# Kernel tuning notes

Hardware: AMD Instinct MI355X
Metric: run time of the kernel (lower is better)

Reference implementation:

```python
import jax, jax.numpy as jnp
import numpy as np

N, E, B, PG = 20000, 320000, 20, 1000  # nodes, edges, graphs, nodes-per-graph
H, L, NB, EI = 256, 6, 16, 8           # hidden, layers, node_base_dim, edge_in_dim
LN_EPS = 1e-5


def setup_inputs() -> dict:
    key = jax.random.key(0)
    ks = jax.random.split(key, 32)
    w = lambda i, s: (jax.random.normal(ks[i], s, jnp.float32) * 0.05)
    inp = {
        "x": jax.random.normal(ks[0], (N, NB), jnp.float32),
        "edge_attr": jax.random.normal(ks[1], (E, EI), jnp.float32),
        "c": jax.random.normal(ks[2], (B, PG), jnp.float32),
        "edge_index": jax.random.randint(ks[3], (2, E), 0, N),
        "node_gid": jnp.arange(N) // PG,   # batch.batch
        "node_lid": jnp.arange(N) % PG,    # node local index
        # edge_mlp: Linear(EI,H), ReLU, Linear(H,H)
        "ew1": w(4, (EI, H)), "eb1": jnp.zeros((H,), jnp.float32),
        "ew2": w(5, (H, H)),  "eb2": jnp.zeros((H,), jnp.float32),
        # input_proj: Linear(NB+1, H), SiLU
        "in_w": w(6, (NB + 1, H)), "in_b": jnp.zeros((H,), jnp.float32),
        # per-layer GINEConv edge lin (edge_dim -> in_channels)
        "lin_w": w(7, (L, H, H)), "lin_b": jnp.zeros((L, H), jnp.float32),
        # per-layer conv MLP: Linear(H,H), SiLU, Linear(H,H)
        "cw1": w(8, (L, H, H)), "cb1": jnp.zeros((L, H), jnp.float32),
        "cw2": w(9, (L, H, H)), "cb2": jnp.zeros((L, H), jnp.float32),
        # per-layer LayerNorm
        "ln_g": jnp.ones((L, H), jnp.float32), "ln_b": jnp.zeros((L, H), jnp.float32),
        # pool_attn: Linear(H,H), Tanh, Linear(H,1)
        "pa_w1": w(10, (H, H)), "pa_b1": jnp.zeros((H,), jnp.float32),
        "pa_w2": w(11, (H, 1)), "pa_b2": jnp.zeros((1,), jnp.float32),
        # head: Linear(H,H), SiLU, Linear(H,1)
        "hw1": w(12, (H, H)), "hb1": jnp.zeros((H,), jnp.float32),
        "hw2": w(13, (H, 1)), "hb2": jnp.zeros((1,), jnp.float32),
    }
    return inp


def _layer_norm(z, g, b):
    m = jnp.mean(z, axis=-1, keepdims=True)
    v = jnp.mean(jnp.square(z - m), axis=-1, keepdims=True)
    return (z - m) * jax.lax.rsqrt(v + LN_EPS) * g + b


def reference(x, edge_attr, c, edge_index, node_gid, node_lid,
              ew1, eb1, ew2, eb2, in_w, in_b,
              lin_w, lin_b, cw1, cb1, cw2, cb2, ln_g, ln_b,
              pa_w1, pa_b1, pa_w2, pa_b2, hw1, hb1, hw2, hb2):
    silu = jax.nn.silu
    # c_scalar: per-node coefficient
    c_scalar = c[node_gid, node_lid][:, None]                       # [N,1]
    xin = jnp.concatenate([x, c_scalar], axis=-1)                   # [N,NB+1]
    e = jax.nn.relu(edge_attr @ ew1 + eb1) @ ew2 + eb2              # [E,H]
    h = silu(xin @ in_w + in_b)                                     # [N,H]
    src, dst = edge_index[0], edge_index[1]
    for l in range(L):
        msg = jax.nn.relu(h[src] + (e @ lin_w[l] + lin_b[l]))       # [E,H]
        agg = jnp.zeros_like(h).at[dst].add(msg)                    # scatter-add
        z = h + agg                                                 # (1+eps)*x_i + agg, eps=0
        h_new = silu(z @ cw1[l] + cb1[l]) @ cw2[l] + cb2[l]
        h_new = _layer_norm(h_new, ln_g[l], ln_b[l])
        h = h + silu(h_new)
    # attention pooling: global softmax over nodes, renormalized per graph
    scores = jnp.tanh(h @ pa_w1 + pa_b1) @ pa_w2 + pa_b2            # [N,1]
    attn = jax.nn.softmax(scores, axis=0)                           # [N,1]
    seg_sum = jax.ops.segment_sum(attn[:, 0], node_gid, num_segments=B)  # [B]
    attn_n = attn[:, 0] / (seg_sum[node_gid] + 1e-8)                # [N]
    pooled = jax.ops.segment_sum(h * attn_n[:, None], node_gid, num_segments=B)  # [B,H]
    q = (silu(pooled @ hw1 + hb1) @ hw2 + hb2)[:, 0]                # [B]
    return q
```

## Files before the change

kernel.cpp:

```cpp
#include <hip/hip_runtime.h>
#include <hip/hip_bf16.h>
#include <cstdint>


#define NN 20000
#define EE 320000
#define BBG 20
#define PGN 1000
#define HH 256
#define LL 6

typedef short bf16x8 __attribute__((ext_vector_type(8)));
typedef float f32x4 __attribute__((ext_vector_type(4)));

__device__ __forceinline__ void async16(const void* g, void* l) {
  __builtin_amdgcn_global_load_lds(
      (const __attribute__((address_space(1))) unsigned int*)(uintptr_t)g,
      (__attribute__((address_space(3))) unsigned int*)(uintptr_t)l, 16, 0, 0);
}

__device__ __forceinline__ float siluf(float x) { return x / (1.f + __expf(-x)); }

__device__ __forceinline__ unsigned int f2bu(float x) {
  __hip_bfloat16 h = __float2bfloat16(x);
  return (unsigned int)*(unsigned short*)&h;
}

__device__ __forceinline__ float b2f(unsigned short u) {
  unsigned int v = ((unsigned int)u) << 16;
  return *(float*)&v;
}

enum { EPI_SILU = 1, EPI_PLAIN = 2, EPI_TANH = 3 };

template <int EPI>
__global__ void __launch_bounds__(256, 2) gemm256(
    const __hip_bfloat16* __restrict__ A, const __hip_bfloat16* __restrict__ Wt,
    const float* __restrict__ bias, int M, float* __restrict__ outf,
    __hip_bfloat16* __restrict__ outb) {
  __shared__ __align__(16) __hip_bfloat16 sA[128 * 32];
  __shared__ __align__(16) __hip_bfloat16 sB[128 * 32];

  const int t = threadIdx.x;
  const int wave = t >> 6, lane = t & 63;
  const int row0 = blockIdx.x * 128;
  const int col0 = blockIdx.y * 128;

  const int wrow = (wave >> 1) * 64;
  const int wcol = (wave & 1) * 64;
  const int fr = lane & 15, q = lane >> 4;

  f32x4 zero = {0.f, 0.f, 0.f, 0.f};
  f32x4 acc[4][4];
#pragma unroll
  for (int i = 0; i < 4; i++)
#pragma unroll
    for (int j = 0; j < 4; j++) acc[i][j] = zero;

  const int c1 = t, c2 = t + 256;
  const int lr1 = c1 >> 2, lr2 = c2 >> 2;
  const int q1 = (c1 & 3) ^ ((lr1 >> 1) & 3);
  const int q2 = (c2 & 3) ^ ((lr2 >> 1) & 3);
  int rA1 = row0 + lr1; if (rA1 >= M) rA1 = M - 1;
  int rA2 = row0 + lr2; if (rA2 >= M) rA2 = M - 1;
  const int rB1 = col0 + lr1, rB2 = col0 + lr2;

  for (int k0 = 0; k0 < 256; k0 += 32) {
    async16((const char*)(A + (size_t)rA1 * HH + k0) + q1 * 16,
            (char*)sA + wave * 1024);
    async16((const char*)(A + (size_t)rA2 * HH + k0) + q2 * 16,
            (char*)sA + 4096 + wave * 1024);
    async16((const char*)(Wt + (size_t)rB1 * HH + k0) + q1 * 16,
            (char*)sB + wave * 1024);
    async16((const char*)(Wt + (size_t)rB2 * HH + k0) + q2 * 16,
            (char*)sB + 4096 + wave * 1024);
    __syncthreads();
    bf16x8 af[4], bfr[4];
#pragma unroll
    for (int i = 0; i < 4; i++) {
      const int row = wrow + i * 16 + fr;
      af[i] = *(const bf16x8*)&sA[row * 32 + ((q ^ ((row >> 1) & 3))) * 8];
    }
#pragma unroll
    for (int j = 0; j < 4; j++) {
      const int row = wcol + j * 16 + fr;
      bfr[j] = *(const bf16x8*)&sB[row * 32 + ((q ^ ((row >> 1) & 3))) * 8];
    }
#pragma unroll
    for (int i = 0; i < 4; i++)
#pragma unroll
      for (int j = 0; j < 4; j++)
        acc[i][j] = __builtin_amdgcn_mfma_f32_16x16x32_bf16(af[i], bfr[j],
                                                            acc[i][j], 0, 0, 0);
    __syncthreads();
  }

#pragma unroll
  for (int j = 0; j < 4; j++) {
    const int col = col0 + wcol + j * 16 + fr;
    const float bs = bias[col];
#pragma unroll
    for (int i = 0; i < 4; i++) {
      const int lr0 = wrow + i * 16 + q * 4;
#pragma unroll
      for (int r = 0; r < 4; r++) {
        const int grow = row0 + lr0 + r;
        float v = acc[i][j][r] + bs;
        if (grow < M) {
          if (EPI == EPI_SILU) {
            outb[(size_t)grow * HH + col] = __float2bfloat16(siluf(v));
          } else if (EPI == EPI_PLAIN) {
            outf[(size_t)grow * HH + col] = v;
          } else {
            outb[(size_t)grow * HH + col] = __float2bfloat16(tanhf(v));
          }
        }
      }
    }
  }
}

__global__ void __launch_bounds__(256, 4) mlp_ln(
    const float* __restrict__ z, const __hip_bfloat16* __restrict__ W1t,
    const float* __restrict__ b1, const __hip_bfloat16* __restrict__ W2t,
    const float* __restrict__ b2, const float* __restrict__ g,
    const float* __restrict__ bbv, float* __restrict__ h,
    float* __restrict__ yzf, __hip_bfloat16* __restrict__ hb) {
  __shared__ __align__(16) char smem[2048 + 16384 + 32 * 264 * 2];
  __hip_bfloat16* sA = (__hip_bfloat16*)smem;
  __hip_bfloat16* sB = (__hip_bfloat16*)(smem + 2048);
  unsigned short* sT = (unsigned short*)(smem + 18432);

  const int t = threadIdx.x;
  const int wave = t >> 6, lane = t & 63;
  const int row0 = blockIdx.x * 32;
  const int fr = lane & 15, q = lane >> 4;
  const int rt = wave & 1;
  const int chf = wave >> 1;

  const int lrA = t >> 2;
  const int qA = (t & 3) ^ ((lrA >> 1) & 3);
  int qB[4], rB[4];
#pragma unroll
  for (int p = 0; p < 4; p++) {
    const int c = t + p * 256;
    const int lr = c >> 2;
    qB[p] = (c & 3) ^ ((lr >> 1) & 3);
    rB[p] = lr;
  }

  f32x4 zero = {0.f, 0.f, 0.f, 0.f};
  f32x4 acc[8];
#pragma unroll
  for (int j = 0; j < 8; j++) acc[j] = zero;

  const int arow = rt * 16 + fr;
  const int aswz = (q ^ ((arow >> 1) & 3)) * 8;

  for (int k0 = 0; k0 < 256; k0 += 32) {
    if (t < 128) {
      const float* s1 = z + (size_t)(row0 + lrA) * HH + k0 + qA * 8;
      float4 a0 = *(const float4*)s1;
      float4 a1 = *(const float4*)(s1 + 4);
      uint4 u;
      u.x = f2bu(a0.x) | (f2bu(a0.y) << 16);
      u.y = f2bu(a0.z) | (f2bu(a0.w) << 16);
      u.z = f2bu(a1.x) | (f2bu(a1.y) << 16);
      u.w = f2bu(a1.z) | (f2bu(a1.w) << 16);
      *(uint4*)((char*)sA + t * 16) = u;
    }
#pragma unroll
    for (int p = 0; p < 4; p++)
      async16((const char*)(W1t + (size_t)rB[p] * HH + k0) + qB[p] * 16,
              (char*)sB + p * 4096 + wave * 1024);
    __syncthreads();
    bf16x8 af = *(const bf16x8*)&sA[arow * 32 + aswz];
#pragma unroll
    for (int j = 0; j < 8; j++) {
      const int row = chf * 128 + j * 16 + fr;
      bf16x8 bfr = *(const bf16x8*)&sB[row * 32 + ((q ^ ((row >> 1) & 3))) * 8];
      acc[j] = __builtin_amdgcn_mfma_f32_16x16x32_bf16(af, bfr, acc[j], 0, 0, 0);
    }
    __syncthreads();
  }
#pragma unroll
  for (int j = 0; j < 8; j++) {
    const int col = chf * 128 + j * 16 + fr;
    const float bs = b1[col];
    const int r0 = rt * 16 + q * 4;
#pragma unroll
    for (int r = 0; r < 4; r++)
      sT[(r0 + r) * 264 + col] = (unsigned short)f2bu(siluf(acc[j][r] + bs));
  }
#pragma unroll
  for (int j = 0; j < 8; j++) acc[j] = zero;

  for (int k0 = 0; k0 < 256; k0 += 32) {
#pragma unroll
    for (int p = 0; p < 4; p++)
      async16((const char*)(W2t + (size_t)rB[p] * HH + k0) + qB[p] * 16,
              (char*)sB + p * 4096 + wave * 1024);
    __syncthreads();
    bf16x8 af = *(const bf16x8*)&sT[arow * 264 + k0 + q * 8];
#pragma unroll
    for (int j = 0; j < 8; j++) {
      const int row = chf * 128 + j * 16 + fr;
      bf16x8 bfr = *(const bf16x8*)&sB[row * 32 + ((q ^ ((row >> 1) & 3))) * 8];
      acc[j] = __builtin_amdgcn_mfma_f32_16x16x32_bf16(af, bfr, acc[j], 0, 0, 0);
    }
    __syncthreads();
  }
#pragma unroll
  for (int j = 0; j < 8; j++) {
    const int col = chf * 128 + j * 16 + fr;
    const float bs = b2[col];
    const int r0 = rt * 16 + q * 4;
#pragma unroll
    for (int r = 0; r < 4; r++)
      sT[(r0 + r) * 264 + col] = (unsigned short)f2bu(acc[j][r] + bs);
  }
  __syncthreads();

  for (int rr = 0; rr < 8; rr++) {
    const int r = wave * 8 + rr;
    const int grow = row0 + r;
    float v[4];
    float s = 0.f;
#pragma unroll
    for (int i = 0; i < 4; i++) {
      v[i] = b2f(sT[r * 264 + lane + i * 64]);
      s += v[i];
    }
#pragma unroll
    for (int o = 32; o; o >>= 1) s += __shfl_xor(s, o);
    const float mean = s * (1.f / 256.f);
    float var = 0.f;
#pragma unroll
    for (int i = 0; i < 4; i++) { float d = v[i] - mean; var += d * d; }
#pragma unroll
    for (int o = 32; o; o >>= 1) var += __shfl_xor(var, o);
    const float rs = rsqrtf(var * (1.f / 256.f) + 1e-5f);
#pragma unroll
    for (int i = 0; i < 4; i++) {
      const int c = lane + i * 64;
      float ln = (v[i] - mean) * rs * g[c] + bbv[c];
      float si = siluf(ln);
      size_t idx = (size_t)grow * HH + c;
      float nh = h[idx] + si;
      h[idx] = nh;
      yzf[idx] = nh;
      hb[idx] = __float2bfloat16(nh);
    }
  }
}

__global__ void __launch_bounds__(256, 4) edge_fused(
    const __hip_bfloat16* __restrict__ te, const __hip_bfloat16* __restrict__ Wt,
    const float* __restrict__ bias, const __hip_bfloat16* __restrict__ hbv,
    const int* __restrict__ srcp, const int* __restrict__ dstp,
    float* __restrict__ z) {
  __shared__ __align__(16) char smem[32768];
  __shared__ int sSrc[128], sDst[128];
  __hip_bfloat16* sA = (__hip_bfloat16*)smem;
  __hip_bfloat16* sB = (__hip_bfloat16*)(smem + 16384);
  unsigned short* sRed = (unsigned short*)smem;

  const int t = threadIdx.x;
  const int wave = t >> 6, lane = t & 63;
  const int row0 = blockIdx.y * 128;
  const int col0 = blockIdx.x * 128;

  if (t < 128) { sSrc[t] = srcp[row0 + t]; sDst[t] = dstp[row0 + t]; }
  __syncthreads();

  const int wrow = (wave >> 1) * 64;
  const int fr = lane & 15, q = lane >> 4;
  const int rc = lane, rb = wave;

  f32x4 zero = {0.f, 0.f, 0.f, 0.f};
  f32x4 acc[4][4];
#pragma unroll
  for (int i = 0; i < 4; i++)
#pragma unroll
    for (int j = 0; j < 4; j++) acc[i][j] = zero;

  const int c1 = t, c2 = t + 256;
  const int lr1 = c1 >> 2, lr2 = c2 >> 2;
  const int q1 = (c1 & 3) ^ ((lr1 >> 1) & 3);
  const int q2 = (c2 & 3) ^ ((lr2 >> 1) & 3);
  const int rA1 = row0 + lr1, rA2 = row0 + lr2;
  const int rB1 = col0 + lr1, rB2 = col0 + lr2;

#pragma unroll
  for (int it = 0; it < 4; it++) {
    const int ka = it * 64, kb = ka + 32;
    async16((const char*)(te + (size_t)rA1 * HH + ka) + q1 * 16,
            (char*)sA + wave * 1024);
    async16((const char*)(te + (size_t)rA2 * HH + ka) + q2 * 16,
            (char*)sA + 4096 + wave * 1024);
    async16((const char*)(te + (size_t)rA1 * HH + kb) + q1 * 16,
            (char*)sA + 8192 + wave * 1024);
    async16((const char*)(te + (size_t)rA2 * HH + kb) + q2 * 16,
            (char*)sA + 12288 + wave * 1024);
    async16((const char*)(Wt + (size_t)rB1 * HH + ka) + q1 * 16,
            (char*)sB + wave * 1024);
    async16((const char*)(Wt + (size_t)rB2 * HH + ka) + q2 * 16,
            (char*)sB + 4096 + wave * 1024);
    async16((const char*)(Wt + (size_t)rB1 * HH + kb) + q1 * 16,
            (char*)sB + 8192 + wave * 1024);
    async16((const char*)(Wt + (size_t)rB2 * HH + kb) + q2 * 16,
            (char*)sB + 12288 + wave * 1024);
    __syncthreads();
#pragma unroll
    for (int half = 0; half < 2; half++) {
      const __hip_bfloat16* pA = sA + half * 4096;
      const __hip_bfloat16* pB = sB + half * 4096;
      bf16x8 af[4], bfr[4];
#pragma unroll
      for (int i = 0; i < 4; i++) {
        const int row = wrow + i * 16 + fr;
        af[i] = *(const bf16x8*)&pA[row * 32 + ((q ^ ((row >> 1) & 3))) * 8];
      }
#pragma unroll
      for (int j = 0; j < 4; j++) {
        const int row = (wave & 1) * 64 + j * 16 + fr;
        bfr[j] = *(const bf16x8*)&pB[row * 32 + ((q ^ ((row >> 1) & 3))) * 8];
      }
#pragma unroll
      for (int i = 0; i < 4; i++)
#pragma unroll
        for (int j = 0; j < 4; j++)
          acc[i][j] = __builtin_amdgcn_mfma_f32_16x16x32_bf16(af[i], bfr[j],
                                                              acc[i][j], 0, 0, 0);
    }
    __syncthreads();
  }

#pragma unroll
  for (int hf = 0; hf < 2; hf++) {
    if ((wave & 1) == hf) {
#pragma unroll
      for (int j = 0; j < 4; j++) {
        const int cl = j * 16 + fr;
        const float bs = bias[col0 + hf * 64 + cl];
#pragma unroll
        for (int i = 0; i < 4; i++) {
          const int r0 = wrow + i * 16 + q * 4;
          f32x4 v = acc[i][j];
          unsigned int p0 = f2bu(v[0] + bs) | (f2bu(v[1] + bs) << 16);
          unsigned int p1 = f2bu(v[2] + bs) | (f2bu(v[3] + bs) << 16);
          *(unsigned int*)&sRed[cl * 130 + r0] = p0;
          *(unsigned int*)&sRed[cl * 130 + r0 + 2] = p1;
        }
      }
    }
    __syncthreads();
    const int gcol = col0 + hf * 64 + rc;
    float a = 0.f;
    int cur = sDst[rb * 32];
    for (int ch = 0; ch < 4; ch++) {
      float hv8[8];
#pragma unroll
      for (int u = 0; u < 8; u++)
        hv8[u] = __bfloat162float(
            hbv[(size_t)sSrc[rb * 32 + ch * 8 + u] * HH + gcol]);
#pragma unroll
      for (int u = 0; u < 8; u++) {
        const int row = rb * 32 + ch * 8 + u;
        const int d = sDst[row];
        if (d != cur) {
          unsafeAtomicAdd(&z[(size_t)cur * HH + gcol], a);
          a = 0.f;
          cur = d;
        }
        float m = b2f(sRed[rc * 130 + row]) + hv8[u];
        a += m > 0.f ? m : 0.f;
      }
    }
    unsafeAtomicAdd(&z[(size_t)cur * HH + gcol], a);
    __syncthreads();
  }
}

__global__ void __launch_bounds__(256) hist_k(const int* __restrict__ edst,
                                              int* __restrict__ cnt) {
  const int e = blockIdx.x * 256 + threadIdx.x;
  if (e < EE) atomicAdd(&cnt[edst[e]], 1);
}

__global__ void __launch_bounds__(256) scan_k(const int* __restrict__ cnt,
                                              int* __restrict__ rowptr) {
  __shared__ int wsum[4];
  __shared__ int carry;
  const int t = threadIdx.x, wave = t >> 6, lane = t & 63;
  if (t == 0) carry = 0;
  __syncthreads();
  for (int base = 0; base < NN; base += 256) {
    const int idx = base + t;
    int v = (idx < NN) ? cnt[idx] : 0;
    int inc = v;
#pragma unroll
    for (int o = 1; o < 64; o <<= 1) {
      int u = __shfl_up(inc, o);
      if (lane >= o) inc += u;
    }
    if (lane == 63) wsum[wave] = inc;
    __syncthreads();
    int woff = 0;
    for (int w2 = 0; w2 < wave; w2++) woff += wsum[w2];
    if (idx < NN) rowptr[idx] = carry + woff + inc - v;
    const int total = wsum[0] + wsum[1] + wsum[2] + wsum[3];
    __syncthreads();
    if (t == 0) carry += total;
    __syncthreads();
  }
  if (t == 0) rowptr[NN] = carry;
}

__global__ void __launch_bounds__(256) scatter_k(
    const int* __restrict__ esrc, const int* __restrict__ edst,
    int* __restrict__ cursor, int* __restrict__ posof,
    int* __restrict__ srcp, int* __restrict__ dstp) {
  const int e = blockIdx.x * 256 + threadIdx.x;
  if (e < EE) {
    const int d = edst[e];
    const int pos = atomicAdd(&cursor[d], 1);
    posof[e] = pos;
    srcp[pos] = esrc[e];
    dstp[pos] = d;
  }
}

__global__ void __launch_bounds__(256) edge_hidden(
    const float* __restrict__ ea, const float* __restrict__ ew1,
    const float* __restrict__ eb1, const int* __restrict__ posof,
    __hip_bfloat16* __restrict__ tout) {
  __shared__ float w[8 * 256];
  __shared__ float b[256];
  __shared__ float sea[16 * 8];
  __shared__ int spos[16];
  const int t = threadIdx.x;
  for (int i = t; i < 8 * 256; i += 256) w[i] = ew1[i];
  b[t] = eb1[t];
  const int e0 = blockIdx.x * 16;
  if (t < 128) sea[t] = ea[(size_t)e0 * 8 + t];
  if (t < 16) spos[t] = posof[e0 + t];
  __syncthreads();
  for (int e = 0; e < 16; e++) {
    float a = b[t];
#pragma unroll
    for (int j = 0; j < 8; j++) a += sea[e * 8 + j] * w[j * 256 + t];
    tout[(size_t)spos[e] * HH + t] = __float2bfloat16(a > 0.f ? a : 0.f);
  }
}

__global__ void __launch_bounds__(256) fold_edge_w(
    const float* __restrict__ ew2, const float* __restrict__ lin_w,
    const float* __restrict__ eb2, const float* __restrict__ lin_b,
    __hip_bfloat16* __restrict__ Wlt, float* __restrict__ bl) {
  const int l = blockIdx.x >> 8, j = blockIdx.x & 255;
  const int c = threadIdx.x;
  __shared__ float row[256];
  row[c] = ew2[j * 256 + c];
  __syncthreads();
  const float* lw = lin_w + (size_t)l * 65536;
  float a = 0.f;
  for (int k = 0; k < 256; k++) a += row[k] * lw[k * 256 + c];
  Wlt[((size_t)l * 256 + c) * 256 + j] = __float2bfloat16(a);
  if (j == 0) {
    float s = lin_b[l * 256 + c];
    for (int k = 0; k < 256; k++) s += eb2[k] * lw[k * 256 + c];
    bl[l * 256 + c] = s;
  }
}

__global__ void __launch_bounds__(256) tcast_all(
    const float* __restrict__ cw1, const float* __restrict__ cw2,
    const float* __restrict__ paw1, __hip_bfloat16* __restrict__ cw1t,
    __hip_bfloat16* __restrict__ cw2t, __hip_bfloat16* __restrict__ paw1t) {
  const int b = blockIdx.x;
  const float* s;
  __hip_bfloat16* d;
  if (b < 1536) { int l = b >> 8; s = cw1 + (size_t)l * 65536; d = cw1t + (size_t)l * 65536; }
  else if (b < 3072) { int l = (b - 1536) >> 8; s = cw2 + (size_t)l * 65536; d = cw2t + (size_t)l * 65536; }
  else { s = paw1; d = paw1t; }
  const int r = b & 255, c = threadIdx.x;
  d[(size_t)c * 256 + r] = __float2bfloat16(s[(size_t)r * 256 + c]);
}

__global__ void __launch_bounds__(256) node_init(
    const float* __restrict__ x, const float* __restrict__ cc,
    const int* __restrict__ gid, const int* __restrict__ lid,
    const float* __restrict__ in_w, const float* __restrict__ in_b,
    float* __restrict__ h, float* __restrict__ yzf,
    __hip_bfloat16* __restrict__ hb) {
  __shared__ float w[17 * 256];
  __shared__ float b[256];
  __shared__ float sx[16 * 17];
  const int t = threadIdx.x;
  for (int i = t; i < 17 * 256; i += 256) w[i] = in_w[i];
  b[t] = in_b[t];
  const int n0 = blockIdx.x * 16;
  sx[(t >> 4) * 17 + (t & 15)] = x[(size_t)(n0 + (t >> 4)) * 16 + (t & 15)];
  if (t < 16) {
    int n = n0 + t;
    sx[t * 17 + 16] = cc[gid[n] * PGN + lid[n]];
  }
  __syncthreads();
  for (int e = 0; e < 16; e++) {
    float a = b[t];
#pragma unroll
    for (int j = 0; j < 17; j++) a += sx[e * 17 + j] * w[j * 256 + t];
    float s = siluf(a);
    size_t idx = (size_t)(n0 + e) * HH + t;
    h[idx] = s;
    yzf[idx] = s;
    hb[idx] = __float2bfloat16(s);
  }
}

__global__ void __launch_bounds__(256) score_k(
    const __hip_bfloat16* __restrict__ s1, const float* __restrict__ pw2,
    const float* __restrict__ pb2, float* __restrict__ scores,
    float* __restrict__ pmax) {
  __shared__ float w2[256];
  __shared__ float bm[4];
  const int t = threadIdx.x, wave = t >> 6, lane = t & 63;
  w2[t] = pw2[t];
  __syncthreads();
  const size_t row = (size_t)blockIdx.x * 4 + wave;
  float a = 0.f;
#pragma unroll
  for (int i = 0; i < 4; i++) {
    int c = lane + i * 64;
    a += __bfloat162float(s1[row * HH + c]) * w2[c];
  }
#pragma unroll
  for (int o = 32; o; o >>= 1) a += __shfl_xor(a, o);
  float sc = a + pb2[0];
  if (lane == 0) { scores[row] = sc; bm[wave] = sc; }
  __syncthreads();
  if (t == 0) pmax[blockIdx.x] = fmaxf(fmaxf(bm[0], bm[1]), fmaxf(bm[2], bm[3]));
}

__global__ void __launch_bounds__(256) gmax_k(const float* __restrict__ pmax,
                                              int n, float* __restrict__ gmax) {
  const int t = threadIdx.x;
  float m = -3.4e38f;
  for (int i = t; i < n; i += 256) m = fmaxf(m, pmax[i]);
#pragma unroll
  for (int o = 32; o; o >>= 1) m = fmaxf(m, __shfl_xor(m, o));
  __shared__ float wm[4];
  if ((t & 63) == 0) wm[t >> 6] = m;
  __syncthreads();
  if (t == 0) gmax[0] = fmaxf(fmaxf(wm[0], wm[1]), fmaxf(wm[2], wm[3]));
}

__global__ void __launch_bounds__(256) esum_k(
    const float* __restrict__ scores, const int* __restrict__ gid,
    const float* __restrict__ gmax, float* __restrict__ en,
    float* __restrict__ seg) {
  __shared__ float ls[BBG + 1];
  const int t = threadIdx.x;
  if (t < BBG + 1) ls[t] = 0.f;
  __syncthreads();
  const int n = blockIdx.x * 256 + t;
  if (n < NN) {
    float e = __expf(scores[n] - gmax[0]);
    en[n] = e;
    atomicAdd(&ls[gid[n]], e);
    atomicAdd(&ls[BBG], e);
  }
  __syncthreads();
  if (t < BBG + 1) unsafeAtomicAdd(&seg[t], ls[t]);
}

__global__ void __launch_bounds__(256) pooled_k(
    const float* __restrict__ h, const float* __restrict__ en,
    const float* __restrict__ seg, float* __restrict__ pooled) {
  const int g = blockIdx.x / 40, ch = blockIdx.x % 40;
  const int c = threadIdx.x;
  const int n0 = g * PGN + ch * 25;
  float a = 0.f;
  for (int i = 0; i < 25; i++) {
    int n = n0 + i;
    a += en[n] * h[(size_t)n * HH + c];
  }
  const float inv = 1.f / (seg[g] + 1e-8f * seg[BBG]);
  unsafeAtomicAdd(&pooled[g * HH + c], a * inv);
}

__global__ void __launch_bounds__(256) head_k(
    const float* __restrict__ pooled, const float* __restrict__ hw1,
    const float* __restrict__ hb1, const float* __restrict__ hw2,
    const float* __restrict__ hb2, float* __restrict__ qout) {
  const int b = blockIdx.x, c = threadIdx.x;
  __shared__ float p[256];
  __shared__ float wsum[4];
  p[c] = pooled[b * 256 + c];
  __syncthreads();
  float a = hb1[c];
  for (int k = 0; k < 256; k++) a += p[k] * hw1[k * 256 + c];
  float v = siluf(a) * hw2[c];
#pragma unroll
  for (int o = 32; o; o >>= 1) v += __shfl_xor(v, o);
  if ((c & 63) == 0) wsum[c >> 6] = v;
  __syncthreads();
  if (c == 0) qout[b] = wsum[0] + wsum[1] + wsum[2] + wsum[3] + hb2[0];
}

extern "C" void kernel_launch(void* const* d_in, const int* in_sizes, int n_in,
                              void* d_out, int out_size, void* d_ws, size_t ws_size,
                              hipStream_t stream) {
  const float* x = (const float*)d_in[0];
  const float* edge_attr = (const float*)d_in[1];
  const float* cc = (const float*)d_in[2];
  const int* edge_index = (const int*)d_in[3];
  const int* node_gid = (const int*)d_in[4];
  const int* node_lid = (const int*)d_in[5];
  const float* ew1 = (const float*)d_in[6];
  const float* eb1 = (const float*)d_in[7];
  const float* ew2 = (const float*)d_in[8];
  const float* eb2 = (const float*)d_in[9];
  const float* in_w = (const float*)d_in[10];
  const float* in_b = (const float*)d_in[11];
  const float* lin_w = (const float*)d_in[12];
  const float* lin_b = (const float*)d_in[13];
  const float* cw1 = (const float*)d_in[14];
  const float* cb1 = (const float*)d_in[15];
  const float* cw2 = (const float*)d_in[16];
  const float* cb2 = (const float*)d_in[17];
  const float* ln_g = (const float*)d_in[18];
  const float* ln_b = (const float*)d_in[19];
  const float* pa_w1 = (const float*)d_in[20];
  const float* pa_b1 = (const float*)d_in[21];
  const float* pa_w2 = (const float*)d_in[22];
  const float* pa_b2 = (const float*)d_in[23];
  const float* hw1 = (const float*)d_in[24];
  const float* hb1 = (const float*)d_in[25];
  const float* hw2 = (const float*)d_in[26];
  const float* hb2 = (const float*)d_in[27];
  float* qout = (float*)d_out;

  char* w = (char*)d_ws;
  auto alloc = [&](size_t bytes) {
    char* p = w;
    w += (bytes + 255) & ~(size_t)255;
    return p;
  };
  __hip_bfloat16* t_e = (__hip_bfloat16*)alloc((size_t)EE * HH * 2);
  float* h = (float*)alloc((size_t)NN * HH * 4);
  float* yzf = (float*)alloc((size_t)NN * HH * 4);
  __hip_bfloat16* hb = (__hip_bfloat16*)alloc((size_t)NN * HH * 2);
  __hip_bfloat16* t2 = (__hip_bfloat16*)alloc((size_t)NN * HH * 2);
  __hip_bfloat16* Wlt = (__hip_bfloat16*)alloc((size_t)LL * HH * HH * 2);
  float* bl = (float*)alloc((size_t)LL * HH * 4);
  __hip_bfloat16* cw1t = (__hip_bfloat16*)alloc((size_t)LL * HH * HH * 2);
  __hip_bfloat16* cw2t = (__hip_bfloat16*)alloc((size_t)LL * HH * HH * 2);
  __hip_bfloat16* paw1t = (__hip_bfloat16*)alloc((size_t)HH * HH * 2);
  float* scores = (float*)alloc((size_t)NN * 4);
  float* pmax = (float*)alloc(5008 * 4);
  float* en = (float*)alloc((size_t)NN * 4);
  float* seg = (float*)alloc((BBG + 1) * 4);
  float* gmax = (float*)alloc(4);
  float* pooled = (float*)alloc((size_t)BBG * HH * 4);
  int* cnt = (int*)alloc((size_t)NN * 4);
  int* rowptr = (int*)alloc((size_t)(NN + 1) * 4);
  int* cursor = (int*)alloc((size_t)NN * 4);
  int* posof = (int*)alloc((size_t)EE * 4);
  int* srcp = (int*)alloc((size_t)EE * 4);
  int* dstp = (int*)alloc((size_t)EE * 4);

  const int* esrc = edge_index;
  const int* edst = edge_index + EE;

  hipMemsetAsync(cnt, 0, (size_t)NN * 4, stream);
  hipMemsetAsync(seg, 0, (BBG + 1) * 4, stream);
  hipMemsetAsync(pooled, 0, (size_t)BBG * HH * 4, stream);

  hist_k<<<(EE + 255) / 256, 256, 0, stream>>>(edst, cnt);
  scan_k<<<1, 256, 0, stream>>>(cnt, rowptr);
  hipMemcpyAsync(cursor, rowptr, (size_t)NN * 4, hipMemcpyDeviceToDevice, stream);
  scatter_k<<<(EE + 255) / 256, 256, 0, stream>>>(esrc, edst, cursor, posof,
                                                  srcp, dstp);

  fold_edge_w<<<LL * 256, 256, 0, stream>>>(ew2, lin_w, eb2, lin_b, Wlt, bl);
  tcast_all<<<3328, 256, 0, stream>>>(cw1, cw2, pa_w1, cw1t, cw2t, paw1t);
  edge_hidden<<<EE / 16, 256, 0, stream>>>(edge_attr, ew1, eb1, posof, t_e);
  node_init<<<NN / 16, 256, 0, stream>>>(x, cc, node_gid, node_lid, in_w, in_b,
                                         h, yzf, hb);

  dim3 gE(2, EE / 128), gN((NN + 127) / 128, 2);
  const int gMLP = NN / 32;
  for (int l = 0; l < LL; l++) {
    edge_fused<<<gE, 256, 0, stream>>>(t_e, Wlt + (size_t)l * HH * HH,
                                       bl + l * HH, hb, srcp, dstp, yzf);
    mlp_ln<<<gMLP, 256, 0, stream>>>(
        yzf, cw1t + (size_t)l * HH * HH, cb1 + l * HH,
        cw2t + (size_t)l * HH * HH, cb2 + l * HH, ln_g + l * HH, ln_b + l * HH,
        h, yzf, hb);
  }

  gemm256<EPI_TANH><<<gN, 256, 0, stream>>>(hb, paw1t, pa_b1, NN, nullptr, t2);
  score_k<<<NN / 4, 256, 0, stream>>>(t2, pa_w2, pa_b2, scores, pmax);
  gmax_k<<<1, 256, 0, stream>>>(pmax, NN / 4, gmax);
  esum_k<<<(NN + 255) / 256, 256, 0, stream>>>(scores, node_gid, gmax, en, seg);
  pooled_k<<<BBG * 40, 256, 0, stream>>>(h, en, seg, pooled);
  head_k<<<BBG, 256, 0, stream>>>(pooled, hw1, hb1, hw2, hb2, qout);
}
```

Before: 1.113 ms.

## Give each wave a private LDS tile to drop block barriers in edge GEMM

The edge_fused GEMM mainloop now has each wave load its own 64-row A and B slices into a private LDS region, so it waits only on its own vmcnt instead of block-wide __syncthreads per K step. K is walked in 8 steps of 32, and the src/dst index loads are split across waves. This removes barrier stalls but duplicates global loads, since A and B slices are each fetched by two waves. There is also no double buffering, so each wave waits on the load of the next step it has just issued.

Measured after the change: 1.258 ms. +13.1%, slower.

```diff
diff --git a/kernel.cpp b/kernel.cpp
--- a/kernel.cpp
+++ b/kernel.cpp
@@ -261,8 +261,6 @@
     float* __restrict__ z) {
   __shared__ __align__(16) char smem[32768];
   __shared__ int sSrc[128], sDst[128];
-  __hip_bfloat16* sA = (__hip_bfloat16*)smem;
-  __hip_bfloat16* sB = (__hip_bfloat16*)(smem + 16384);
   unsigned short* sRed = (unsigned short*)smem;
 
   const int t = threadIdx.x;
@@ -270,13 +268,28 @@
   const int row0 = blockIdx.y * 128;
   const int col0 = blockIdx.x * 128;
 
-  if (t < 128) { sSrc[t] = srcp[row0 + t]; sDst[t] = dstp[row0 + t]; }
-  __syncthreads();
-
-  const int wrow = (wave >> 1) * 64;
+  if (lane < 32) sSrc[wave * 32 + lane] = srcp[row0 + wave * 32 + lane];
+  else sDst[wave * 32 + lane - 32] = dstp[row0 + wave * 32 + lane - 32];
+
+  const int wr = (wave >> 1) * 64;
+  const int wc = (wave & 1) * 64;
   const int fr = lane & 15, q = lane >> 4;
   const int rc = lane, rb = wave;
 
+  __hip_bfloat16* sAw = (__hip_bfloat16*)(smem + wave * 4096);
+  __hip_bfloat16* sBw = (__hip_bfloat16*)(smem + 16384 + wave * 4096);
+
+  const char* gA[4];
+  const char* gB[4];
+#pragma unroll
+  for (int p = 0; p < 4; p++) {
+    const int c = p * 64 + lane;
+    const int row = c >> 2;
+    const int qq = (c & 3) ^ ((row >> 1) & 3);
+    gA[p] = (const char*)(te + (size_t)(row0 + wr + row) * HH) + qq * 16;
+    gB[p] = (const char*)(Wt + (size_t)(col0 + wc + row) * HH) + qq * 16;
+  }
+
   f32x4 zero = {0.f, 0.f, 0.f, 0.f};
   f32x4 acc[4][4];
 #pragma unroll
@@ -284,57 +297,44 @@
 #pragma unroll
     for (int j = 0; j < 4; j++) acc[i][j] = zero;
 
-  const int c1 = t, c2 = t + 256;
-  const int lr1 = c1 >> 2, lr2 = c2 >> 2;
-  const int q1 = (c1 & 3) ^ ((lr1 >> 1) & 3);
-  const int q2 = (c2 & 3) ^ ((lr2 >> 1) & 3);
-  const int rA1 = row0 + lr1, rA2 = row0 + lr2;
-  const int rB1 = col0 + lr1, rB2 = col0 + lr2;
-
-#pragma unroll
-  for (int it = 0; it < 4; it++) {
-    const int ka = it * 64, kb = ka + 32;
-    async16((const char*)(te + (size_t)rA1 * HH + ka) + q1 * 16,
-            (char*)sA + wave * 1024);
-    async16((const char*)(te + (size_t)rA2 * HH + ka) + q2 * 16,
-            (char*)sA + 4096 + wave * 1024);
-    async16((const char*)(te + (size_t)rA1 * HH + kb) + q1 * 16,
-            (char*)sA + 8192 + wave * 1024);
-    async16((const char*)(te + (size_t)rA2 * HH + kb) + q2 * 16,
-            (char*)sA + 12288 + wave * 1024);
-    async16((const char*)(Wt + (size_t)rB1 * HH + ka) + q1 * 16,
-            (char*)sB + wave * 1024);
-    async16((const char*)(Wt + (size_t)rB2 * HH + ka) + q2 * 16,
-            (char*)sB + 4096 + wave * 1024);
-    async16((const char*)(Wt + (size_t)rB1 * HH + kb) + q1 * 16,
-            (char*)sB + 8192 + wave * 1024);
-    async16((const char*)(Wt + (size_t)rB2 * HH + kb) + q2 * 16,
-            (char*)sB + 12288 + wave * 1024);
-    __syncthreads();
-#pragma unroll
-    for (int half = 0; half < 2; half++) {
-      const __hip_bfloat16* pA = sA + half * 4096;
-      const __hip_bfloat16* pB = sB + half * 4096;
-      bf16x8 af[4], bfr[4];
-#pragma unroll
-      for (int i = 0; i < 4; i++) {
-        const int row = wrow + i * 16 + fr;
-        af[i] = *(const bf16x8*)&pA[row * 32 + ((q ^ ((row >> 1) & 3))) * 8];
+#pragma unroll
+  for (int p = 0; p < 4; p++) {
+    async16(gA[p], (char*)sAw + p * 1024);
+    async16(gB[p], (char*)sBw + p * 1024);
+  }
+
+#pragma unroll
+  for (int it = 0; it < 8; it++) {
+    asm volatile("s_waitcnt vmcnt(0)" ::: "memory");
+    bf16x8 af[4], bfr[4];
+#pragma unroll
+    for (int i = 0; i < 4; i++) {
+      const int row = i * 16 + fr;
+      af[i] = *(const bf16x8*)&sAw[row * 32 + ((q ^ ((row >> 1) & 3))) * 8];
+    }
+#pragma unroll
+    for (int j = 0; j < 4; j++) {
+      const int row = j * 16 + fr;
+      bfr[j] = *(const bf16x8*)&sBw[row * 32 + ((q ^ ((row >> 1) & 3))) * 8];
+    }
+#pragma unroll
+    for (int i = 0; i < 4; i++)
+#pragma unroll
+      for (int j = 0; j < 4; j++)
+        acc[i][j] = __builtin_amdgcn_mfma_f32_16x16x32_bf16(af[i], bfr[j],
+                                                            acc[i][j], 0, 0, 0);
+    asm volatile("" ::: "memory");
+    if (it < 7) {
+      const int off = (it + 1) * 64;
+#pragma unroll
+      for (int p = 0; p < 4; p++) {
+        async16(gA[p] + off, (char*)sAw + p * 1024);
+        async16(gB[p] + off, (char*)sBw + p * 1024);
       }
-#pragma unroll
-      for (int j = 0; j < 4; j++) {
-        const int row = (wave & 1) * 64 + j * 16 + fr;
-        bfr[j] = *(const bf16x8*)&pB[row * 32 + ((q ^ ((row >> 1) & 3))) * 8];
-      }
-#pragma unroll
-      for (int i = 0; i < 4; i++)
-#pragma unroll
-        for (int j = 0; j < 4; j++)
-          acc[i][j] = __builtin_amdgcn_mfma_f32_16x16x32_bf16(af[i], bfr[j],
-                                                              acc[i][j], 0, 0, 0);
-    }
-    __syncthreads();
-  }
+    }
+  }
+
+  __syncthreads();
 
 #pragma unroll
   for (int hf = 0; hf < 2; hf++) {
@@ -345,7 +345,7 @@
         const float bs = bias[col0 + hf * 64 + cl];
 #pragma unroll
         for (int i = 0; i < 4; i++) {
-          const int r0 = wrow + i * 16 + q * 4;
+          const int r0 = wr + i * 16 + q * 4;
           f32x4 v = acc[i][j];
           unsigned int p0 = f2bu(v[0] + bs) | (f2bu(v[1] + bs) << 16);
           unsigned int p1 = f2bu(v[2] + bs) | (f2bu(v[3] + bs) << 16);
```
